# Kernel tuning notes

Hardware: AMD Instinct MI355X
Metric: run time of the kernel (lower is better)

Reference implementation:

```python
import jax, jax.numpy as jnp
import numpy as np

TOPK = 13
NUM_CLASSES = 80
ALPHA = 1.0
BETA = 3.0
EPS = 1e-9
K_NEAR = 4
N_BINS = 36  # theta bins: arange(0, 360, 10)


def _dist_max_per_bin(anc_points, gt_pts):
    """gt_pts: (bs,nm,360,2), anc_points: (na,2) -> (bs,nm,na,36) ray targets."""
    d = gt_pts[:, :, None, :, :] - anc_points[None, None, :, None, :]  # (bs,nm,na,360,2)
    dist = jnp.sqrt(jnp.sum(d * d, axis=-1))                           # (bs,nm,na,360)
    ang = jnp.rad2deg(jnp.arctan2(d[..., 1], d[..., 0])) % 360.0       # (bs,nm,na,360)
    theta = jnp.arange(0, 360, 360 // N_BINS).astype(ang.dtype)        # (36,)

    def per_theta(th):
        diff = jnp.abs(ang - th)
        diff = jnp.where(diff > 180.0, 360.0 - diff, diff)
        neg_v, idx = jax.lax.top_k(-diff, K_NEAR)   # 4 nearest-angle contour pts
        val = -neg_v
        dk = jnp.take_along_axis(dist, idx, axis=-1)
        dk = jnp.where(jnp.min(val, axis=-1, keepdims=True) > 3.0, 1e-6, dk)
        return jnp.max(dk, axis=-1)                 # (bs,nm,na)

    dm = jax.lax.map(per_theta, theta)              # (36,bs,nm,na); chunked to bound memory
    return jnp.maximum(jnp.moveaxis(dm, 0, -1), 1e-6)


def _mask_iou(target, pred):
    l_max = jnp.maximum(target, pred)
    l_min = jnp.maximum(jnp.minimum(target, pred), 1e-6)
    return jnp.sum(l_min, -1) / jnp.sum(l_max, -1)


def _forward(pd_scores, pd_bboxes, anc_points, gt_labels, gt_bboxes, mask_gt, gt_coor):
    bs, na, nc = pd_scores.shape
    nm = gt_bboxes.shape[1]
    gl = gt_labels[..., 0]            # (bs,nm) int
    mgt = mask_gt[..., 0]             # (bs,nm) float
    gt_pts = gt_coor.reshape(bs, nm, 360, 2)

    # select_candidates_in_gts: anchor center strictly inside gt box
    lt, rb = gt_bboxes[..., :2], gt_bboxes[..., 2:]
    deltas = jnp.concatenate([anc_points[None, None] - lt[:, :, None],
                              rb[:, :, None] - anc_points[None, None]], axis=-1)
    mask_in_gts = (jnp.min(deltas, -1) > 1e-9).astype(pd_scores.dtype)  # (bs,nm,na)
    mask_sel = (mask_in_gts * mgt[:, :, None]) > 0

    # get_box_metrics_polar (dense over (bs,nm,na) instead of boolean-mask select)
    dist_max = _dist_max_per_bin(anc_points, gt_pts)                    # (bs,nm,na,36)
    overlaps = jnp.where(mask_sel, _mask_iou(dist_max, pd_bboxes[:, None]), 0.0)
    bbox_scores = jnp.take_along_axis(jnp.swapaxes(pd_scores, 1, 2), gl[:, :, None], axis=1)
    bbox_scores = jnp.where(mask_sel, bbox_scores, 0.0)
    align_metric = (bbox_scores ** ALPHA) * (overlaps ** BETA)

    # select_topk_candidates
    _, topk_idxs = jax.lax.top_k(align_metric, TOPK)
    topk_idxs = jnp.where(mgt[:, :, None] > 0, topk_idxs, 0)
    count = jnp.sum(jax.nn.one_hot(topk_idxs, na, dtype=align_metric.dtype), axis=-2)
    mask_topk = jnp.where(count > 1, 0.0, count)
    mask_pos = mask_topk * mask_in_gts * mgt[:, :, None]

    # select_highest_overlaps
    fg = jnp.sum(mask_pos, -2)                                          # (bs,na)
    multi = fg[:, None, :] > 1
    is_max = jnp.moveaxis(jax.nn.one_hot(jnp.argmax(overlaps, 1), nm, dtype=mask_pos.dtype), -1, 1)
    mask_pos = jnp.where(multi, is_max, mask_pos)
    fg_mask = jnp.sum(mask_pos, -2)
    target_gt_idx = jnp.argmax(mask_pos, -2)                            # (bs,na)

    # per-positive ray-distance targets + polar centerness (dense, masked)
    mask_pos_b = mask_pos > 0
    gt_dist = jnp.where(mask_pos_b[..., None], dist_max, 0.0)           # (bs,nm,na,36)
    cent = jnp.sqrt(jnp.min(dist_max, -1) / jnp.max(dist_max, -1))
    centerness_gt = jnp.where(mask_pos_b, cent, 0.0)                    # (bs,nm,na)

    # get_targets
    target_labels = jnp.maximum(jnp.take_along_axis(gl, target_gt_idx, axis=1), 0)
    target_bboxes = jnp.take_along_axis(gt_bboxes, target_gt_idx[..., None], axis=1)
    target_scores = jax.nn.one_hot(target_labels, NUM_CLASSES, dtype=pd_scores.dtype)
    target_scores = jnp.where((fg_mask > 0)[..., None], target_scores, 0.0)

    am = align_metric * mask_pos
    pos_align = jnp.max(am, -1, keepdims=True)
    pos_ov = jnp.max(overlaps * mask_pos, -1, keepdims=True)
    norm_align = jnp.max(am * pos_ov / (pos_align + EPS), -2)[..., None]  # (bs,na,1)
    target_scores = target_scores * norm_align

    return (target_labels, target_bboxes, target_scores, mask_pos_b,
            target_gt_idx, gt_dist, centerness_gt, fg_mask > 0)


def setup_inputs():
    key = jax.random.key(0)
    k = jax.random.split(key, 6)
    bs, nc, nm = 2, 80, 10
    pts, strs = [], []
    for s in (8, 16, 32):  # 640x640 YOLO grid -> 8400 anchors
        n = 640 // s
        yv, xv = np.meshgrid(np.arange(n), np.arange(n), indexing='ij')
        pts.append(np.stack([(xv + 0.5) * s, (yv + 0.5) * s], -1).reshape(-1, 2))
        strs.append(np.full((pts[-1].shape[0], 1), s, dtype=np.float32))
    anc_points = jnp.asarray(np.concatenate(pts).astype(np.float32))
    stride_tensor = jnp.asarray(np.concatenate(strs))
    na = anc_points.shape[0]
    pd_scores = jax.random.uniform(k[0], (bs, na, nc), dtype=jnp.float32)
    pd_bboxes = jax.random.uniform(k[1], (bs, na, 36), dtype=jnp.float32) * 100.0 + 1.0
    gt_labels = jax.random.randint(k[2], (bs, nm, 1), 0, nc)
    ctr = jax.random.uniform(k[3], (bs, nm, 2), dtype=jnp.float32) * 440.0 + 100.0
    wh = jax.random.uniform(k[4], (bs, nm, 2), dtype=jnp.float32) * 140.0 + 40.0
    gt_bboxes = jnp.concatenate([ctr - wh / 2.0, ctr + wh / 2.0], -1)
    th = jnp.arange(360.0) * (jnp.pi / 180.0)
    rad = (jnp.min(wh, -1, keepdims=True) / 2.0) * (0.6 + 0.4 * jax.random.uniform(k[5], (bs, nm, 360), dtype=jnp.float32))
    ray = jnp.stack([jnp.cos(th), jnp.sin(th)], -1)  # (360,2)
    gt_coor = (ctr[:, :, None, :] + rad[..., None] * ray[None, None]).reshape(bs, nm, 720)
    mask_gt = jnp.ones((bs, nm, 1), dtype=jnp.float32).at[1, 7:].set(0.0)
    return dict(pd_scores=pd_scores, pd_bboxes=pd_bboxes, anc_points=anc_points,
                gt_labels=gt_labels, gt_bboxes=gt_bboxes, mask_gt=mask_gt,
                gt_coor=gt_coor, stride_tensor=stride_tensor, ss=640,
                gt_center=ctr, imgsz=640)


def reference(pd_scores, pd_bboxes, anc_points, gt_labels, gt_bboxes, mask_gt, gt_coor, stride_tensor, ss, gt_center, imgsz):
    # ss, gt_center, imgsz, stride_tensor are accepted (as in the torch signature) but unused
    return _forward(pd_scores, pd_bboxes, anc_points, gt_labels, gt_bboxes, mask_gt, gt_coor)
```

## Files before the change

### kernel.cpp

```cpp
#include <hip/hip_runtime.h>

#define BS 2
#define NM 10
#define NA 8400
#define NC 80
#define NBIN 36
#define KTOP 13
#define NRECT (BS*NM*3)

__device__ __forceinline__ void rect_one(int bm, int lv,
    const float* __restrict__ gtb, const float* __restrict__ mgt,
    int& x0, int& y0, int& cx, int& cnt, int& n, int& base){
  cnt = 0; x0 = 0; y0 = 0; cx = 0; n = 0; base = 0;
  if (mgt[bm] > 0.f){
    float s = (float)(8 << lv);
    n = 640 >> (3 + lv);
    base = (lv == 0) ? 0 : ((lv == 1) ? 6400 : 8000);
    float lx = gtb[bm*4+0], ly = gtb[bm*4+1];
    float rx = gtb[bm*4+2], ry = gtb[bm*4+3];
    int a0 = (int)ceilf(lx/s - 0.5f); a0 = min(max(a0, 0), n);
    while (a0 > 0   &&  (((a0-1)+0.5f)*s - lx > 1e-9f)) a0--;
    while (a0 < n   && !(((a0  )+0.5f)*s - lx > 1e-9f)) a0++;
    int a1 = (int)floorf(rx/s - 0.5f); a1 = min(max(a1, -1), n-1);
    while (a1 < n-1 &&  (rx - ((a1+1)+0.5f)*s > 1e-9f)) a1++;
    while (a1 >= 0  && !(rx - ((a1  )+0.5f)*s > 1e-9f)) a1--;
    int b0 = (int)ceilf(ly/s - 0.5f); b0 = min(max(b0, 0), n);
    while (b0 > 0   &&  (((b0-1)+0.5f)*s - ly > 1e-9f)) b0--;
    while (b0 < n   && !(((b0  )+0.5f)*s - ly > 1e-9f)) b0++;
    int b1 = (int)floorf(ry/s - 0.5f); b1 = min(max(b1, -1), n-1);
    while (b1 < n-1 &&  (ry - ((b1+1)+0.5f)*s > 1e-9f)) b1++;
    while (b1 >= 0  && !(ry - ((b1  )+0.5f)*s > 1e-9f)) b1--;
    cx = max(0, a1 - a0 + 1);
    int cy = max(0, b1 - b0 + 1);
    cnt = cx * cy;
    x0 = a0; y0 = b0;
  }
}

__device__ __forceinline__ void rect_setup(int tid,
    const float* __restrict__ gtb, const float* __restrict__ mgt,
    int* sx0, int* sy0, int* scx, int* scum, int* sn, int* sbase){
  if (tid < NRECT){
    int bm = tid/3, lv = tid - bm*3;
    int x0, y0, cx, cnt, n, base;
    rect_one(bm, lv, gtb, mgt, x0, y0, cx, cnt, n, base);
    sx0[tid] = x0; sy0[tid] = y0; scx[tid] = cx;
    scum[tid] = cnt; sn[tid] = n; sbase[tid] = base;
  }
  __syncthreads();
  if (tid == 0){
    int acc = 0;
    for (int r = 0; r < NRECT; r++){ int c = scum[r]; scum[r] = acc; acc += c; }
    scum[NRECT] = acc;
  }
  __syncthreads();
}

__device__ __forceinline__ int pair_from_p(int p,
    const int* sx0, const int* sy0, const int* scx,
    const int* scum, const int* sn, const int* sbase){
  int r = 0;
  while (r < NRECT-1 && scum[r+1] <= p) r++;
  int idx = p - scum[r];
  int cx = scx[r];
  int yi = idx / cx;
  int xi = idx - yi*cx;
  int a = sbase[r] + (sy0[r] + yi)*sn[r] + (sx0[r] + xi);
  int bm = r/3;
  return bm*NA + a;
}

__global__ void k_zero(float* __restrict__ out, float* __restrict__ wf){
  float4 z = make_float4(0.f,0.f,0.f,0.f);
  int gsz = gridDim.x*256, gtid = blockIdx.x*256 + threadIdx.x;
  float4* a = (float4*)(out + 84000);
  for (int i = gtid; i < 1344000/4; i += gsz) a[i] = z;
  float4* b = (float4*)(out + 1612800);
  for (int i = gtid; i < (6048000+168000)/4; i += gsz) b[i] = z;
  float4* c = (float4*)(wf + 16);
  for (int i = gtid; i < (3*BS*NM*NA + 40)/4; i += gsz) c[i] = z;
}

__global__ __launch_bounds__(256)
void k_dist(const float* __restrict__ pds, const float* __restrict__ pdb,
            const float* __restrict__ anc, const int* __restrict__ gl,
            const float* __restrict__ gtb, const float* __restrict__ mgt,
            const float* __restrict__ coor,
            float* __restrict__ out, float* __restrict__ wf){
  float* o_gtdist  = out + 1612800;
  float* w_align = wf + 16;
  float* w_ovl   = w_align + BS*NM*NA;

  __shared__ int sx0[NRECT], sy0[NRECT], scx[NRECT], scum[NRECT+1], sn[NRECT], sbase[NRECT];
  __shared__ float2 s_da[360];
  __shared__ float  s_m[NBIN*49];

  int tid = threadIdx.x;
  int lane = tid & 63, wave = tid >> 6;

  rect_setup(tid, gtb, mgt, sx0, sy0, scx, scum, sn, sbase);
  int total = scum[NRECT];

  int id = tid;
  int bin = id % 36;
  int chunk = id / 36;
  bool act = (id < 216);
  float th = (float)(bin*10);

  for (int p = blockIdx.x; p < total; p += gridDim.x){
    int t = pair_from_p(p, sx0, sy0, scx, scum, sn, sbase);
    int a = t % NA; int bm = t / NA; int b = bm / NM;
    float ax = anc[2*a], ay = anc[2*a+1];
    const float* cc = coor + bm*720;
    for (int i = tid; i < 360; i += 256){
      float dx = cc[2*i]   - ax;
      float dy = cc[2*i+1] - ay;
      float dist = sqrtf(dx*dx + dy*dy);
      float an = atan2f(dy, dx) * 57.29577951308232f;
      if (an < 0.f) an += 360.f;
      s_da[i] = make_float2(dist, an);
    }
    __syncthreads();
    if (act){
      float v0=1e30f, v1=1e30f, v2=1e30f, v3=1e30f;
      float d0=0.f, d1=0.f, d2=0.f, d3=0.f;
      int base = chunk*60;
      for (int k = 0; k < 60; k++){
        float2 da = s_da[base + k];
        float diff = fabsf(da.y - th);
        diff = fminf(diff, 360.f - diff);
        if (diff < v3){
          v3 = diff; d3 = da.x;
          if (v3 < v2){ float tv=v2; v2=v3; v3=tv; float td=d2; d2=d3; d3=td; }
          if (v2 < v1){ float tv=v1; v1=v2; v2=tv; float td=d1; d1=d2; d2=td; }
          if (v1 < v0){ float tv=v0; v0=v1; v1=tv; float td=d0; d0=d1; d1=td; }
        }
      }
      int mb = bin*49 + chunk*8;
      s_m[mb+0]=v0; s_m[mb+1]=v1; s_m[mb+2]=v2; s_m[mb+3]=v3;
      s_m[mb+4]=d0; s_m[mb+5]=d1; s_m[mb+6]=d2; s_m[mb+7]=d3;
    }
    __syncthreads();
    if (wave == 0){
      float sum_min = 0.f, sum_max = 0.f;
      if (lane < NBIN){
        int mb = lane*49;
        float h0=s_m[mb+0], h1=s_m[mb+8],  h2=s_m[mb+16],
              h3=s_m[mb+24], h4=s_m[mb+32], h5=s_m[mb+40];
        int p0=0, p1=0, p2=0, p3=0, p4=0, p5=0;
        float v0m = 0.f, dmax = 0.f;
#pragma unroll
        for (int step = 0; step < 4; step++){
          float bv = h0; int bw = 0;
          if (h1 < bv){ bv = h1; bw = 1; }
          if (h2 < bv){ bv = h2; bw = 2; }
          if (h3 < bv){ bv = h3; bw = 3; }
          if (h4 < bv){ bv = h4; bw = 4; }
          if (h5 < bv){ bv = h5; bw = 5; }
          float dd;
          if (bw == 0){ dd = s_m[mb+ 4+p0]; p0++; h0 = (p0<4)? s_m[mb   +p0] : 1e30f; }
          else if (bw == 1){ dd = s_m[mb+12+p1]; p1++; h1 = (p1<4)? s_m[mb+ 8+p1] : 1e30f; }
          else if (bw == 2){ dd = s_m[mb+20+p2]; p2++; h2 = (p2<4)? s_m[mb+16+p2] : 1e30f; }
          else if (bw == 3){ dd = s_m[mb+28+p3]; p3++; h3 = (p3<4)? s_m[mb+24+p3] : 1e30f; }
          else if (bw == 4){ dd = s_m[mb+36+p4]; p4++; h4 = (p4<4)? s_m[mb+32+p4] : 1e30f; }
          else             { dd = s_m[mb+44+p5]; p5++; h5 = (p5<4)? s_m[mb+40+p5] : 1e30f; }
          if (step == 0) v0m = bv;
          dmax = fmaxf(dmax, dd);
        }
        float dm = (v0m > 3.0f) ? 1e-6f : dmax;
        float dfin = fmaxf(dm, 1e-6f);
        o_gtdist[(size_t)t*NBIN + lane] = dfin;
        float pr = pdb[((size_t)b*NA + a)*NBIN + lane];
        sum_max = fmaxf(dfin, pr);
        sum_min = fmaxf(fminf(dfin, pr), 1e-6f);
      }
      for (int off = 32; off > 0; off >>= 1){
        sum_min += __shfl_down(sum_min, off);
        sum_max += __shfl_down(sum_max, off);
      }
      if (lane == 0){
        float ov = sum_min / sum_max;
        int cls = gl[bm];
        float sc = pds[((size_t)b*NA + a)*NC + cls];
        w_align[t] = sc * ov * ov * ov;
        w_ovl[t]   = ov;
      }
    }
    __syncthreads();
  }
}

__global__ __launch_bounds__(256)
void k_topk(const float* __restrict__ gtb, const float* __restrict__ mgt,
            const float* __restrict__ w_align, float* __restrict__ w_mask){
  int bm = blockIdx.x;
  const float* al = w_align + (size_t)bm*NA;
  int tid = threadIdx.x;
  __shared__ int rx0[3], ry0[3], rcx[3], rcum[4], rn[3], rbase[3];
  __shared__ float sv[256*KTOP];
  __shared__ int   si[256*KTOP];
  __shared__ float wv4[4];
  __shared__ int   wi4[4];

  if (tid < 3){
    int x0, y0, cx, cnt, n, base;
    rect_one(bm, tid, gtb, mgt, x0, y0, cx, cnt, n, base);
    rx0[tid]=x0; ry0[tid]=y0; rcx[tid]=cx; rcum[tid]=cnt; rn[tid]=n; rbase[tid]=base;
  }
  __syncthreads();
  if (tid == 0){
    int acc = 0;
#pragma unroll
    for (int r = 0; r < 3; r++){ int c = rcum[r]; rcum[r] = acc; acc += c; }
    rcum[3] = acc;
  }
  __syncthreads();
  int total = rcum[3];

  float v[KTOP]; int ix[KTOP];
#pragma unroll
  for (int j = 0; j < KTOP; j++){ v[j] = -1.f; ix[j] = 0x7fffffff; }
  for (int p = tid; p < total; p += 256){
    int r = (p >= rcum[1]) + (p >= rcum[2]);
    int idx = p - rcum[r];
    int cx = rcx[r];
    int yi = idx / cx;
    int xi = idx - yi*cx;
    int a = rbase[r] + (ry0[r] + yi)*rn[r] + (rx0[r] + xi);
    float x = al[a];
    if (x > v[KTOP-1]){
      v[KTOP-1] = x; ix[KTOP-1] = a;
#pragma unroll
      for (int j = KTOP-1; j > 0; j--){
        if (v[j] > v[j-1]){
          float tv = v[j-1]; v[j-1] = v[j]; v[j] = tv;
          int   ti = ix[j-1]; ix[j-1] = ix[j]; ix[j] = ti;
        }
      }
    }
  }
#pragma unroll
  for (int j = 0; j < KTOP; j++){ sv[tid*KTOP+j] = v[j]; si[tid*KTOP+j] = ix[j]; }

  int head = 0;
  int lane = tid & 63, wave = tid >> 6;
  for (int r = 0; r < KTOP; r++){
    float cv = sv[tid*KTOP + head];
    int   ci = si[tid*KTOP + head];
    float rv = cv; int ri = ci;
    for (int off = 32; off > 0; off >>= 1){
      float ov = __shfl_down(rv, off);
      int   oi = __shfl_down(ri, off);
      if (ov > rv || (ov == rv && oi < ri)){ rv = ov; ri = oi; }
    }
    if (lane == 0){ wv4[wave] = rv; wi4[wave] = ri; }
    __syncthreads();
    float Wv = wv4[0]; int Wi = wi4[0];
#pragma unroll
    for (int w = 1; w < 4; w++){
      float ov = wv4[w]; int oi = wi4[w];
      if (ov > Wv || (ov == Wv && oi < Wi)){ Wv = ov; Wi = oi; }
    }
    if (ci == Wi && head < KTOP-1) head++;
    if (tid == 0 && Wv > 0.f) w_mask[(size_t)bm*NA + Wi] = 1.f;
    __syncthreads();
  }
}

__global__ void k_final(const float* __restrict__ w_align, const float* __restrict__ w_ovl,
                        float* __restrict__ w_mask,
                        const int* __restrict__ gl, const float* __restrict__ gtb,
                        float* __restrict__ o_labels, float* __restrict__ o_bboxes,
                        float* __restrict__ o_maskpos, float* __restrict__ o_gtidx,
                        float* __restrict__ o_fg,
                        float* __restrict__ w_pa, float* __restrict__ w_po){
  int t = blockIdx.x*256 + threadIdx.x;
  if (t >= BS*NA) return;
  int a = t % NA, b = t / NA;
  float mp[NM];
  int fg = 0;
#pragma unroll
  for (int m = 0; m < NM; m++){
    mp[m] = w_mask[((size_t)(b*NM+m))*NA + a];
    fg += (mp[m] > 0.f) ? 1 : 0;
  }
  if (fg > 1){
    float bv = -1.f; int bi = 0;
#pragma unroll
    for (int m = 0; m < NM; m++){
      float v = w_ovl[((size_t)(b*NM+m))*NA + a];
      if (v > bv){ bv = v; bi = m; }
    }
#pragma unroll
    for (int m = 0; m < NM; m++){
      mp[m] = (m == bi) ? 1.f : 0.f;
      w_mask[((size_t)(b*NM+m))*NA + a] = mp[m];
    }
    fg = 1;
  }
  int tgt = 0;
#pragma unroll
  for (int m = NM-1; m >= 0; m--) if (mp[m] > 0.f) tgt = m;
#pragma unroll
  for (int m = 0; m < NM; m++) o_maskpos[((size_t)(b*NM+m))*NA + a] = mp[m];
  o_gtidx[t] = (float)tgt;
  o_fg[t] = (fg > 0) ? 1.f : 0.f;
  int lbl = gl[b*NM + tgt]; if (lbl < 0) lbl = 0;
  o_labels[t] = (float)lbl;
  const float* bx = gtb + (b*NM + tgt)*4;
  ((float4*)o_bboxes)[t] = make_float4(bx[0], bx[1], bx[2], bx[3]);
  if (fg > 0){
    int bmx = b*NM + tgt;
    float av  = w_align[(size_t)bmx*NA + a];
    float ovv = w_ovl[(size_t)bmx*NA + a];
    atomicMax((unsigned int*)&w_pa[bmx], __float_as_uint(av));
    atomicMax((unsigned int*)&w_po[bmx], __float_as_uint(ovv));
  }
}

#define NB_FIX 512
__global__ void k_fuse(const float* __restrict__ gtb, const float* __restrict__ mgt,
                       const float* __restrict__ w_mask, float* __restrict__ o_gtdist,
                       float* __restrict__ o_cent,
                       const float* __restrict__ w_align,
                       const float* __restrict__ w_pa, const float* __restrict__ w_po,
                       const float* __restrict__ o_labels, const float* __restrict__ o_fg,
                       const float* __restrict__ o_gtidx, float* __restrict__ o_scores){
  if (blockIdx.x < NB_FIX){
    __shared__ int sx0[NRECT], sy0[NRECT], scx[NRECT], scum[NRECT+1], sn[NRECT], sbase[NRECT];
    int tid = threadIdx.x;
    rect_setup(tid, gtb, mgt, sx0, sy0, scx, scum, sn, sbase);
    int total = scum[NRECT];
    int lane = tid & 63, wave = tid >> 6;
    for (int p = blockIdx.x*4 + wave; p < total; p += NB_FIX*4){
      int t = pair_from_p(p, sx0, sy0, scx, scum, sn, sbase);
      float m = w_mask[t];
      float* row = o_gtdist + (size_t)t*NBIN;
      if (m > 0.f){
        float vmin = 1e30f, vmax = 0.f;
        if (lane < NBIN){
          float v = row[lane];
          vmin = v; vmax = v;
        }
        for (int off = 32; off > 0; off >>= 1){
          vmin = fminf(vmin, __shfl_down(vmin, off));
          vmax = fmaxf(vmax, __shfl_down(vmax, off));
        }
        if (lane == 0) o_cent[t] = sqrtf(vmin / vmax);
      } else {
        if (lane < NBIN) row[lane] = 0.f;
      }
    }
  } else {
    int t = (blockIdx.x - NB_FIX)*256 + threadIdx.x;
    if (t < BS*NA && o_fg[t] > 0.f){
      int a = t % NA, b = t / NA;
      int m = (int)o_gtidx[t];
      int bm = b*NM + m;
      float av = w_align[(size_t)bm*NA + a];
      float norm = av * w_po[bm] / (w_pa[bm] + 1e-9f);
      int lbl = (int)o_labels[t];
      o_scores[(size_t)t*NC + lbl] = norm;
    }
  }
}

extern "C" void kernel_launch(void* const* d_in, const int* in_sizes, int n_in,
                              void* d_out, int out_size, void* d_ws, size_t ws_size,
                              hipStream_t stream){
  const float* pds  = (const float*)d_in[0];
  const float* pdb  = (const float*)d_in[1];
  const float* anc  = (const float*)d_in[2];
  const int*   gl   = (const int*)  d_in[3];
  const float* gtb  = (const float*)d_in[4];
  const float* mgt  = (const float*)d_in[5];
  const float* coor = (const float*)d_in[6];

  float* out = (float*)d_out;
  float* o_labels  = out;
  float* o_bboxes  = o_labels + BS*NA;
  float* o_scores  = o_bboxes + BS*NA*4;
  float* o_maskpos = o_scores + (size_t)BS*NA*NC;
  float* o_gtidx   = o_maskpos + BS*NM*NA;
  float* o_gtdist  = o_gtidx + BS*NA;
  float* o_cent    = o_gtdist + (size_t)BS*NM*NA*NBIN;
  float* o_fg      = o_cent + BS*NM*NA;

  float* wf      = (float*)d_ws;
  float* w_align = wf + 16;
  float* w_ovl   = w_align + BS*NM*NA;
  float* w_mask  = w_ovl + BS*NM*NA;
  float* w_pa    = w_mask + BS*NM*NA;
  float* w_po    = w_pa + BS*NM;

  k_zero<<<2048, 256, 0, stream>>>(out, wf);
  k_dist<<<4096, 256, 0, stream>>>(pds, pdb, anc, gl, gtb, mgt, coor, out, wf);
  k_topk<<<BS*NM, 256, 0, stream>>>(gtb, mgt, w_align, w_mask);
  k_final<<<(BS*NA+255)/256, 256, 0, stream>>>(w_align, w_ovl, w_mask, gl, gtb,
                                               o_labels, o_bboxes, o_maskpos, o_gtidx, o_fg,
                                               w_pa, w_po);
  k_fuse<<<NB_FIX + (BS*NA+255)/256, 256, 0, stream>>>(gtb, mgt, w_mask,
                                                       o_gtdist, o_cent,
                                                       w_align, w_pa, w_po,
                                                       o_labels, o_fg, o_gtidx, o_scores);
}
```

Measured before the change: 170.4 us.

## Bucket contour points by angle bin and search only neighbouring bins per wave

The per-anchor ray-distance kernel now handles one (gt, anchor) pair per wavefront instead of per block, which removes block-wide barriers. Contour points are counting-sorted into 10-degree angle buckets in shared memory. Each bin's top-4 nearest-angle search then scans only the adjacent buckets, and falls back to a full 360-point scan when the fourth-best angular distance is not provably within range. Ties are broken by packing the point index into a 64-bit key so the selection matches the reference's index order. This adds shared-memory atomics, a prefix scan and a fallback path, and the grid size is reduced.

```diff
diff --git a/kernel.cpp b/kernel.cpp
--- a/kernel.cpp
+++ b/kernel.cpp
@@ -92,101 +92,118 @@
   float* w_ovl   = w_align + BS*NM*NA;
 
   __shared__ int sx0[NRECT], sy0[NRECT], scx[NRECT], scum[NRECT+1], sn[NRECT], sbase[NRECT];
-  __shared__ float2 s_da[360];
-  __shared__ float  s_m[NBIN*49];
+  __shared__ float2 s_ad[4][360];
+  __shared__ unsigned short s_ix[4][360];
+  __shared__ int s_cnt[4][NBIN];
+  __shared__ int s_off[4][NBIN+1];
+  __shared__ int s_cur[4][NBIN];
 
   int tid = threadIdx.x;
-  int lane = tid & 63, wave = tid >> 6;
+  int lane = tid & 63, wv = tid >> 6;
 
   rect_setup(tid, gtb, mgt, sx0, sy0, scx, scum, sn, sbase);
   int total = scum[NRECT];
 
-  int id = tid;
-  int bin = id % 36;
-  int chunk = id / 36;
-  bool act = (id < 216);
-  float th = (float)(bin*10);
-
-  for (int p = blockIdx.x; p < total; p += gridDim.x){
+  for (int p = blockIdx.x*4 + wv; p < total; p += gridDim.x*4){
     int t = pair_from_p(p, sx0, sy0, scx, scum, sn, sbase);
-    int a = t % NA; int bm = t / NA; int b = bm / NM;
+    int a = t % NA; int bm = t / NA; int bb = bm / NM;
     float ax = anc[2*a], ay = anc[2*a+1];
-    const float* cc = coor + bm*720;
-    for (int i = tid; i < 360; i += 256){
-      float dx = cc[2*i]   - ax;
-      float dy = cc[2*i+1] - ay;
-      float dist = sqrtf(dx*dx + dy*dy);
-      float an = atan2f(dy, dx) * 57.29577951308232f;
-      if (an < 0.f) an += 360.f;
-      s_da[i] = make_float2(dist, an);
-    }
-    __syncthreads();
-    if (act){
-      float v0=1e30f, v1=1e30f, v2=1e30f, v3=1e30f;
-      float d0=0.f, d1=0.f, d2=0.f, d3=0.f;
-      int base = chunk*60;
-      for (int k = 0; k < 60; k++){
-        float2 da = s_da[base + k];
-        float diff = fabsf(da.y - th);
-        diff = fminf(diff, 360.f - diff);
-        if (diff < v3){
-          v3 = diff; d3 = da.x;
-          if (v3 < v2){ float tv=v2; v2=v3; v3=tv; float td=d2; d2=d3; d3=td; }
-          if (v2 < v1){ float tv=v1; v1=v2; v2=tv; float td=d1; d1=d2; d2=td; }
-          if (v1 < v0){ float tv=v0; v0=v1; v1=tv; float td=d0; d0=d1; d1=td; }
+    const float2* cc = (const float2*)(coor + bm*720);
+
+    if (lane < NBIN) s_cnt[wv][lane] = 0;
+
+    float angR[6], dstR[6]; int buR[6];
+#pragma unroll
+    for (int r = 0; r < 6; r++){
+      int i = r*64 + lane;
+      angR[r] = 0.f; dstR[r] = 0.f; buR[r] = -1;
+      if (i < 360){
+        float2 cxy = cc[i];
+        float dx = cxy.x - ax;
+        float dy = cxy.y - ay;
+        float dist = sqrtf(dx*dx + dy*dy);
+        float an = atan2f(dy, dx) * 57.29577951308232f;
+        if (an < 0.f) an += 360.f;
+        int bu = (int)(an * 0.1f); bu = min(bu, NBIN-1);
+        angR[r] = an; dstR[r] = dist; buR[r] = bu;
+        atomicAdd(&s_cnt[wv][bu], 1);
+      }
+    }
+    int c = (lane < NBIN) ? s_cnt[wv][lane] : 0;
+    int incl = c;
+#pragma unroll
+    for (int st = 1; st < 64; st <<= 1){
+      int o = __shfl_up(incl, st);
+      if (lane >= st) incl += o;
+    }
+    if (lane < NBIN){ s_off[wv][lane+1] = incl; s_cur[wv][lane] = incl - c; }
+    if (lane == 0) s_off[wv][0] = 0;
+#pragma unroll
+    for (int r = 0; r < 6; r++){
+      if (buR[r] >= 0){
+        int pos = atomicAdd(&s_cur[wv][buR[r]], 1);
+        s_ad[wv][pos] = make_float2(angR[r], dstR[r]);
+        s_ix[wv][pos] = (unsigned short)(r*64 + lane);
+      }
+    }
+
+    float sum_min = 0.f, sum_max = 0.f;
+    if (lane < NBIN){
+      float th = (float)(lane*10);
+      int r0s, r0e, r1s, r1e;
+      if (lane == 0)      { r0s = s_off[wv][35]; r0e = s_off[wv][36]; r1s = 0; r1e = s_off[wv][2]; }
+      else if (lane == 35){ r0s = s_off[wv][34]; r0e = s_off[wv][36]; r1s = 0; r1e = s_off[wv][1]; }
+      else                { r0s = s_off[wv][lane-1]; r0e = s_off[wv][lane+2]; r1s = 0; r1e = 0; }
+
+      unsigned long long k0,k1,k2,k3;
+      float p0,p1,p2,p3;
+      k0=k1=k2=k3=0xFFFFFFFFFFFFFFFFull;
+      p0=p1=p2=p3=0.f;
+#define EVAL(J) { \
+        float2 ad = s_ad[wv][J]; \
+        unsigned int ixv = s_ix[wv][J]; \
+        float df = fabsf(ad.x - th); \
+        df = fminf(df, 360.f - df); \
+        unsigned long long key = ((unsigned long long)__float_as_uint(df) << 32) | ixv; \
+        if (key < k3){ \
+          k3 = key; p3 = ad.y; \
+          if (k3 < k2){ unsigned long long tk=k2; k2=k3; k3=tk; float tp=p2; p2=p3; p3=tp; } \
+          if (k2 < k1){ unsigned long long tk=k1; k1=k2; k2=tk; float tp=p1; p1=p2; p2=tp; } \
+          if (k1 < k0){ unsigned long long tk=k0; k0=k1; k1=tk; float tp=p0; p0=p1; p1=tp; } \
+        } }
+      for (int j = r0s; j < r0e; j++) EVAL(j)
+      for (int j = r1s; j < r1e; j++) EVAL(j)
+
+      float m  = __uint_as_float((unsigned int)(k0 >> 32));
+      float d4 = __uint_as_float((unsigned int)(k3 >> 32));
+      float res;
+      if (!(m <= 3.0f)){
+        res = 1e-6f;
+      } else {
+        if (!(d4 <= 9.99f)){
+          k0=k1=k2=k3=0xFFFFFFFFFFFFFFFFull;
+          p0=p1=p2=p3=0.f;
+          for (int j = 0; j < 360; j++) EVAL(j)
         }
+        res = fmaxf(fmaxf(fmaxf(p0,p1),fmaxf(p2,p3)), 1e-6f);
       }
-      int mb = bin*49 + chunk*8;
-      s_m[mb+0]=v0; s_m[mb+1]=v1; s_m[mb+2]=v2; s_m[mb+3]=v3;
-      s_m[mb+4]=d0; s_m[mb+5]=d1; s_m[mb+6]=d2; s_m[mb+7]=d3;
-    }
-    __syncthreads();
-    if (wave == 0){
-      float sum_min = 0.f, sum_max = 0.f;
-      if (lane < NBIN){
-        int mb = lane*49;
-        float h0=s_m[mb+0], h1=s_m[mb+8],  h2=s_m[mb+16],
-              h3=s_m[mb+24], h4=s_m[mb+32], h5=s_m[mb+40];
-        int p0=0, p1=0, p2=0, p3=0, p4=0, p5=0;
-        float v0m = 0.f, dmax = 0.f;
-#pragma unroll
-        for (int step = 0; step < 4; step++){
-          float bv = h0; int bw = 0;
-          if (h1 < bv){ bv = h1; bw = 1; }
-          if (h2 < bv){ bv = h2; bw = 2; }
-          if (h3 < bv){ bv = h3; bw = 3; }
-          if (h4 < bv){ bv = h4; bw = 4; }
-          if (h5 < bv){ bv = h5; bw = 5; }
-          float dd;
-          if (bw == 0){ dd = s_m[mb+ 4+p0]; p0++; h0 = (p0<4)? s_m[mb   +p0] : 1e30f; }
-          else if (bw == 1){ dd = s_m[mb+12+p1]; p1++; h1 = (p1<4)? s_m[mb+ 8+p1] : 1e30f; }
-          else if (bw == 2){ dd = s_m[mb+20+p2]; p2++; h2 = (p2<4)? s_m[mb+16+p2] : 1e30f; }
-          else if (bw == 3){ dd = s_m[mb+28+p3]; p3++; h3 = (p3<4)? s_m[mb+24+p3] : 1e30f; }
-          else if (bw == 4){ dd = s_m[mb+36+p4]; p4++; h4 = (p4<4)? s_m[mb+32+p4] : 1e30f; }
-          else             { dd = s_m[mb+44+p5]; p5++; h5 = (p5<4)? s_m[mb+40+p5] : 1e30f; }
-          if (step == 0) v0m = bv;
-          dmax = fmaxf(dmax, dd);
-        }
-        float dm = (v0m > 3.0f) ? 1e-6f : dmax;
-        float dfin = fmaxf(dm, 1e-6f);
-        o_gtdist[(size_t)t*NBIN + lane] = dfin;
-        float pr = pdb[((size_t)b*NA + a)*NBIN + lane];
-        sum_max = fmaxf(dfin, pr);
-        sum_min = fmaxf(fminf(dfin, pr), 1e-6f);
-      }
-      for (int off = 32; off > 0; off >>= 1){
-        sum_min += __shfl_down(sum_min, off);
-        sum_max += __shfl_down(sum_max, off);
-      }
-      if (lane == 0){
-        float ov = sum_min / sum_max;
-        int cls = gl[bm];
-        float sc = pds[((size_t)b*NA + a)*NC + cls];
-        w_align[t] = sc * ov * ov * ov;
-        w_ovl[t]   = ov;
-      }
-    }
-    __syncthreads();
+      o_gtdist[(size_t)t*NBIN + lane] = res;
+      float pr = pdb[((size_t)bb*NA + a)*NBIN + lane];
+      sum_max = fmaxf(res, pr);
+      sum_min = fmaxf(fminf(res, pr), 1e-6f);
+    }
+#undef EVAL
+    for (int off = 32; off > 0; off >>= 1){
+      sum_min += __shfl_down(sum_min, off);
+      sum_max += __shfl_down(sum_max, off);
+    }
+    if (lane == 0){
+      float ov = sum_min / sum_max;
+      int cls = gl[bm];
+      float sc = pds[((size_t)bb*NA + a)*NC + cls];
+      w_align[t] = sc * ov * ov * ov;
+      w_ovl[t]   = ov;
+    }
   }
 }
 
@@ -394,7 +411,7 @@
   float* w_po    = w_pa + BS*NM;
 
   k_zero<<<2048, 256, 0, stream>>>(out, wf);
-  k_dist<<<4096, 256, 0, stream>>>(pds, pdb, anc, gl, gtb, mgt, coor, out, wf);
+  k_dist<<<1536, 256, 0, stream>>>(pds, pdb, anc, gl, gtb, mgt, coor, out, wf);
   k_topk<<<BS*NM, 256, 0, stream>>>(gtb, mgt, w_align, w_mask);
   k_final<<<(BS*NA+255)/256, 256, 0, stream>>>(w_align, w_ovl, w_mask, gl, gtb,
                                                o_labels, o_bboxes, o_maskpos, o_gtidx, o_fg,
```

Measured after the change: 217.9 us. +27.9%, slower.

## Merge topk, final, and fuse kernels into one cooperative kernel with grid sync

Applied to the files above, without the earlier changes.

The three tail kernels (per-GT top-k selection, per-anchor mask resolution, and gtdist/score fixup) are combined into one cooperative kernel of 256 blocks that uses grid.sync() between phases. This removes two kernel launches and their inter-kernel gaps. In exchange, the top-k phase runs on only 20 of the 256 blocks while the rest wait at the barrier, the fixup loop now strides over 256 blocks instead of 512, and a cooperative launch adds its own overhead.

```diff
diff --git a/kernel.cpp b/kernel.cpp
--- a/kernel.cpp
+++ b/kernel.cpp
@@ -1,4 +1,6 @@
 #include <hip/hip_runtime.h>
+#include <hip/hip_cooperative_groups.h>
+namespace cg = cooperative_groups;
 
 #define BS 2
 #define NM 10
@@ -191,148 +193,145 @@
 }
 
 __global__ __launch_bounds__(256)
-void k_topk(const float* __restrict__ gtb, const float* __restrict__ mgt,
-            const float* __restrict__ w_align, float* __restrict__ w_mask){
-  int bm = blockIdx.x;
-  const float* al = w_align + (size_t)bm*NA;
+void k_tail(const float* __restrict__ gtb, const float* __restrict__ mgt,
+            const float* __restrict__ w_align, const float* __restrict__ w_ovl,
+            float* __restrict__ w_mask,
+            const int* __restrict__ gl,
+            float* __restrict__ o_labels, float* __restrict__ o_bboxes,
+            float* __restrict__ o_maskpos, float* __restrict__ o_gtidx,
+            float* __restrict__ o_fg,
+            float* __restrict__ w_pa, float* __restrict__ w_po,
+            float* __restrict__ o_gtdist, float* __restrict__ o_cent,
+            float* __restrict__ o_scores){
+  cg::grid_group grid = cg::this_grid();
   int tid = threadIdx.x;
+  int lane = tid & 63, wave = tid >> 6;
+
   __shared__ int rx0[3], ry0[3], rcx[3], rcum[4], rn[3], rbase[3];
   __shared__ float sv[256*KTOP];
   __shared__ int   si[256*KTOP];
   __shared__ float wv4[4];
   __shared__ int   wi4[4];
-
-  if (tid < 3){
-    int x0, y0, cx, cnt, n, base;
-    rect_one(bm, tid, gtb, mgt, x0, y0, cx, cnt, n, base);
-    rx0[tid]=x0; ry0[tid]=y0; rcx[tid]=cx; rcum[tid]=cnt; rn[tid]=n; rbase[tid]=base;
-  }
-  __syncthreads();
-  if (tid == 0){
-    int acc = 0;
-#pragma unroll
-    for (int r = 0; r < 3; r++){ int c = rcum[r]; rcum[r] = acc; acc += c; }
-    rcum[3] = acc;
-  }
-  __syncthreads();
-  int total = rcum[3];
-
-  float v[KTOP]; int ix[KTOP];
-#pragma unroll
-  for (int j = 0; j < KTOP; j++){ v[j] = -1.f; ix[j] = 0x7fffffff; }
-  for (int p = tid; p < total; p += 256){
-    int r = (p >= rcum[1]) + (p >= rcum[2]);
-    int idx = p - rcum[r];
-    int cx = rcx[r];
-    int yi = idx / cx;
-    int xi = idx - yi*cx;
-    int a = rbase[r] + (ry0[r] + yi)*rn[r] + (rx0[r] + xi);
-    float x = al[a];
-    if (x > v[KTOP-1]){
-      v[KTOP-1] = x; ix[KTOP-1] = a;
-#pragma unroll
-      for (int j = KTOP-1; j > 0; j--){
-        if (v[j] > v[j-1]){
-          float tv = v[j-1]; v[j-1] = v[j]; v[j] = tv;
-          int   ti = ix[j-1]; ix[j-1] = ix[j]; ix[j] = ti;
-        }
-      }
-    }
-  }
-#pragma unroll
-  for (int j = 0; j < KTOP; j++){ sv[tid*KTOP+j] = v[j]; si[tid*KTOP+j] = ix[j]; }
-
-  int head = 0;
-  int lane = tid & 63, wave = tid >> 6;
-  for (int r = 0; r < KTOP; r++){
-    float cv = sv[tid*KTOP + head];
-    int   ci = si[tid*KTOP + head];
-    float rv = cv; int ri = ci;
-    for (int off = 32; off > 0; off >>= 1){
-      float ov = __shfl_down(rv, off);
-      int   oi = __shfl_down(ri, off);
-      if (ov > rv || (ov == rv && oi < ri)){ rv = ov; ri = oi; }
-    }
-    if (lane == 0){ wv4[wave] = rv; wi4[wave] = ri; }
+  if (blockIdx.x < BS*NM){
+    int bm = blockIdx.x;
+    const float* al = w_align + (size_t)bm*NA;
+    if (tid < 3){
+      int x0, y0, cx, cnt, n, base;
+      rect_one(bm, tid, gtb, mgt, x0, y0, cx, cnt, n, base);
+      rx0[tid]=x0; ry0[tid]=y0; rcx[tid]=cx; rcum[tid]=cnt; rn[tid]=n; rbase[tid]=base;
+    }
     __syncthreads();
-    float Wv = wv4[0]; int Wi = wi4[0];
-#pragma unroll
-    for (int w = 1; w < 4; w++){
-      float ov = wv4[w]; int oi = wi4[w];
-      if (ov > Wv || (ov == Wv && oi < Wi)){ Wv = ov; Wi = oi; }
-    }
-    if (ci == Wi && head < KTOP-1) head++;
-    if (tid == 0 && Wv > 0.f) w_mask[(size_t)bm*NA + Wi] = 1.f;
+    if (tid == 0){
+      int acc = 0;
+#pragma unroll
+      for (int r = 0; r < 3; r++){ int c = rcum[r]; rcum[r] = acc; acc += c; }
+      rcum[3] = acc;
+    }
     __syncthreads();
-  }
-}
-
-__global__ void k_final(const float* __restrict__ w_align, const float* __restrict__ w_ovl,
-                        float* __restrict__ w_mask,
-                        const int* __restrict__ gl, const float* __restrict__ gtb,
-                        float* __restrict__ o_labels, float* __restrict__ o_bboxes,
-                        float* __restrict__ o_maskpos, float* __restrict__ o_gtidx,
-                        float* __restrict__ o_fg,
-                        float* __restrict__ w_pa, float* __restrict__ w_po){
-  int t = blockIdx.x*256 + threadIdx.x;
-  if (t >= BS*NA) return;
-  int a = t % NA, b = t / NA;
-  float mp[NM];
-  int fg = 0;
-#pragma unroll
-  for (int m = 0; m < NM; m++){
-    mp[m] = w_mask[((size_t)(b*NM+m))*NA + a];
-    fg += (mp[m] > 0.f) ? 1 : 0;
-  }
-  if (fg > 1){
-    float bv = -1.f; int bi = 0;
-#pragma unroll
-    for (int m = 0; m < NM; m++){
-      float v = w_ovl[((size_t)(b*NM+m))*NA + a];
-      if (v > bv){ bv = v; bi = m; }
-    }
-#pragma unroll
-    for (int m = 0; m < NM; m++){
-      mp[m] = (m == bi) ? 1.f : 0.f;
-      w_mask[((size_t)(b*NM+m))*NA + a] = mp[m];
-    }
-    fg = 1;
-  }
-  int tgt = 0;
-#pragma unroll
-  for (int m = NM-1; m >= 0; m--) if (mp[m] > 0.f) tgt = m;
-#pragma unroll
-  for (int m = 0; m < NM; m++) o_maskpos[((size_t)(b*NM+m))*NA + a] = mp[m];
-  o_gtidx[t] = (float)tgt;
-  o_fg[t] = (fg > 0) ? 1.f : 0.f;
-  int lbl = gl[b*NM + tgt]; if (lbl < 0) lbl = 0;
-  o_labels[t] = (float)lbl;
-  const float* bx = gtb + (b*NM + tgt)*4;
-  ((float4*)o_bboxes)[t] = make_float4(bx[0], bx[1], bx[2], bx[3]);
-  if (fg > 0){
-    int bmx = b*NM + tgt;
-    float av  = w_align[(size_t)bmx*NA + a];
-    float ovv = w_ovl[(size_t)bmx*NA + a];
-    atomicMax((unsigned int*)&w_pa[bmx], __float_as_uint(av));
-    atomicMax((unsigned int*)&w_po[bmx], __float_as_uint(ovv));
-  }
-}
-
-#define NB_FIX 512
-__global__ void k_fuse(const float* __restrict__ gtb, const float* __restrict__ mgt,
-                       const float* __restrict__ w_mask, float* __restrict__ o_gtdist,
-                       float* __restrict__ o_cent,
-                       const float* __restrict__ w_align,
-                       const float* __restrict__ w_pa, const float* __restrict__ w_po,
-                       const float* __restrict__ o_labels, const float* __restrict__ o_fg,
-                       const float* __restrict__ o_gtidx, float* __restrict__ o_scores){
-  if (blockIdx.x < NB_FIX){
+    int total = rcum[3];
+
+    float v[KTOP]; int ix[KTOP];
+#pragma unroll
+    for (int j = 0; j < KTOP; j++){ v[j] = -1.f; ix[j] = 0x7fffffff; }
+    for (int p = tid; p < total; p += 256){
+      int r = (p >= rcum[1]) + (p >= rcum[2]);
+      int idx = p - rcum[r];
+      int cx = rcx[r];
+      int yi = idx / cx;
+      int xi = idx - yi*cx;
+      int a = rbase[r] + (ry0[r] + yi)*rn[r] + (rx0[r] + xi);
+      float x = al[a];
+      if (x > v[KTOP-1]){
+        v[KTOP-1] = x; ix[KTOP-1] = a;
+#pragma unroll
+        for (int j = KTOP-1; j > 0; j--){
+          if (v[j] > v[j-1]){
+            float tv = v[j-1]; v[j-1] = v[j]; v[j] = tv;
+            int   ti = ix[j-1]; ix[j-1] = ix[j]; ix[j] = ti;
+          }
+        }
+      }
+    }
+#pragma unroll
+    for (int j = 0; j < KTOP; j++){ sv[tid*KTOP+j] = v[j]; si[tid*KTOP+j] = ix[j]; }
+
+    int head = 0;
+    for (int r = 0; r < KTOP; r++){
+      float cv = sv[tid*KTOP + head];
+      int   ci = si[tid*KTOP + head];
+      float rv = cv; int ri = ci;
+      for (int off = 32; off > 0; off >>= 1){
+        float ov = __shfl_down(rv, off);
+        int   oi = __shfl_down(ri, off);
+        if (ov > rv || (ov == rv && oi < ri)){ rv = ov; ri = oi; }
+      }
+      if (lane == 0){ wv4[wave] = rv; wi4[wave] = ri; }
+      __syncthreads();
+      float Wv = wv4[0]; int Wi = wi4[0];
+#pragma unroll
+      for (int w = 1; w < 4; w++){
+        float ov = wv4[w]; int oi = wi4[w];
+        if (ov > Wv || (ov == Wv && oi < Wi)){ Wv = ov; Wi = oi; }
+      }
+      if (ci == Wi && head < KTOP-1) head++;
+      if (tid == 0 && Wv > 0.f) w_mask[(size_t)bm*NA + Wi] = 1.f;
+      __syncthreads();
+    }
+  }
+  grid.sync();
+
+  {
+    int t = blockIdx.x*256 + tid;
+    if (t < BS*NA){
+      int a = t % NA, b = t / NA;
+      float mp[NM];
+      int fg = 0;
+#pragma unroll
+      for (int m = 0; m < NM; m++){
+        mp[m] = w_mask[((size_t)(b*NM+m))*NA + a];
+        fg += (mp[m] > 0.f) ? 1 : 0;
+      }
+      if (fg > 1){
+        float bv = -1.f; int bi = 0;
+#pragma unroll
+        for (int m = 0; m < NM; m++){
+          float v = w_ovl[((size_t)(b*NM+m))*NA + a];
+          if (v > bv){ bv = v; bi = m; }
+        }
+#pragma unroll
+        for (int m = 0; m < NM; m++){
+          mp[m] = (m == bi) ? 1.f : 0.f;
+          w_mask[((size_t)(b*NM+m))*NA + a] = mp[m];
+        }
+        fg = 1;
+      }
+      int tgt = 0;
+#pragma unroll
+      for (int m = NM-1; m >= 0; m--) if (mp[m] > 0.f) tgt = m;
+#pragma unroll
+      for (int m = 0; m < NM; m++) o_maskpos[((size_t)(b*NM+m))*NA + a] = mp[m];
+      o_gtidx[t] = (float)tgt;
+      o_fg[t] = (fg > 0) ? 1.f : 0.f;
+      int lbl = gl[b*NM + tgt]; if (lbl < 0) lbl = 0;
+      o_labels[t] = (float)lbl;
+      const float* bx = gtb + (b*NM + tgt)*4;
+      ((float4*)o_bboxes)[t] = make_float4(bx[0], bx[1], bx[2], bx[3]);
+      if (fg > 0){
+        int bmx = b*NM + tgt;
+        float av  = w_align[(size_t)bmx*NA + a];
+        float ovv = w_ovl[(size_t)bmx*NA + a];
+        atomicMax((unsigned int*)&w_pa[bmx], __float_as_uint(av));
+        atomicMax((unsigned int*)&w_po[bmx], __float_as_uint(ovv));
+      }
+    }
+  }
+  grid.sync();
+
+  {
     __shared__ int sx0[NRECT], sy0[NRECT], scx[NRECT], scum[NRECT+1], sn[NRECT], sbase[NRECT];
-    int tid = threadIdx.x;
     rect_setup(tid, gtb, mgt, sx0, sy0, scx, scum, sn, sbase);
     int total = scum[NRECT];
-    int lane = tid & 63, wave = tid >> 6;
-    for (int p = blockIdx.x*4 + wave; p < total; p += NB_FIX*4){
+    for (int p = blockIdx.x*4 + wave; p < total; p += gridDim.x*4){
       int t = pair_from_p(p, sx0, sy0, scx, scum, sn, sbase);
       float m = w_mask[t];
       float* row = o_gtdist + (size_t)t*NBIN;
@@ -351,8 +350,7 @@
         if (lane < NBIN) row[lane] = 0.f;
       }
     }
-  } else {
-    int t = (blockIdx.x - NB_FIX)*256 + threadIdx.x;
+    int t = blockIdx.x*256 + tid;
     if (t < BS*NA && o_fg[t] > 0.f){
       int a = t % NA, b = t / NA;
       int m = (int)o_gtidx[t];
@@ -395,12 +393,14 @@
 
   k_zero<<<2048, 256, 0, stream>>>(out, wf);
   k_dist<<<4096, 256, 0, stream>>>(pds, pdb, anc, gl, gtb, mgt, coor, out, wf);
-  k_topk<<<BS*NM, 256, 0, stream>>>(gtb, mgt, w_align, w_mask);
-  k_final<<<(BS*NA+255)/256, 256, 0, stream>>>(w_align, w_ovl, w_mask, gl, gtb,
-                                               o_labels, o_bboxes, o_maskpos, o_gtidx, o_fg,
-                                               w_pa, w_po);
-  k_fuse<<<NB_FIX + (BS*NA+255)/256, 256, 0, stream>>>(gtb, mgt, w_mask,
-                                                       o_gtdist, o_cent,
-                                                       w_align, w_pa, w_po,
-                                                       o_labels, o_fg, o_gtidx, o_scores);
-}
+
+  void* args[] = {
+    (void*)&gtb, (void*)&mgt, (void*)&w_align, (void*)&w_ovl, (void*)&w_mask,
+    (void*)&gl,
+    (void*)&o_labels, (void*)&o_bboxes, (void*)&o_maskpos, (void*)&o_gtidx,
+    (void*)&o_fg,
+    (void*)&w_pa, (void*)&w_po,
+    (void*)&o_gtdist, (void*)&o_cent, (void*)&o_scores
+  };
+  hipLaunchCooperativeKernel((void*)k_tail, dim3(256), dim3(256), args, 0, stream);
+}
```

New measurement: 236.1 us. 1.39x slower.
